# Performance work log

Measured on AMD Instinct MI355X. Metric: run time of the kernel, lower is better.

Reference implementation:

```python
import jax, jax.numpy as jnp
import numpy as np

Z_DIM = 3
H = 128
N_BLOCKS = 4
N = 30000
E = 180000
T = 2


def _mlp2(x, W1, b1, W2, b2):
    return jnp.maximum(x @ W1 + b1, 0.0) @ W2 + b2


def _stats(x, eps=1e-8):
    # batch mean/std as accumulated by the running-stat Normalizer (buffers -> no grad)
    m = x.mean(0)
    v = jnp.maximum((x * x).mean(0) - m * m, 0.0)
    s = jnp.maximum(jnp.sqrt(v), eps)
    return jax.lax.stop_gradient(m), jax.lax.stop_gradient(s)


def setup_inputs() -> dict:
    key = jax.random.key(0)
    ks = jax.random.split(key, 32)

    def w(k, shape, fan_in):
        return jax.random.normal(k, shape, jnp.float32) / np.sqrt(fan_in).astype(np.float32)

    inp = {}
    inp["z"] = jax.random.normal(ks[0], (T, N, Z_DIM), jnp.float32)
    inp["z_target"] = jax.random.normal(ks[1], (N, Z_DIM), jnp.float32)
    inp["pos"] = jax.random.uniform(ks[2], (N, 2), jnp.float32)
    # encoder node MLP: z_dim -> H -> H
    inp["enc_node_W1"] = w(ks[3], (Z_DIM, H), Z_DIM)
    inp["enc_node_b1"] = jnp.zeros((H,), jnp.float32)
    inp["enc_node_W2"] = w(ks[4], (H, H), H)
    inp["enc_node_b2"] = jnp.zeros((H,), jnp.float32)
    # encoder edge MLP: edge_dim(3) -> H -> H
    inp["enc_edge_W1"] = w(ks[5], (3, H), 3)
    inp["enc_edge_b1"] = jnp.zeros((H,), jnp.float32)
    inp["enc_edge_W2"] = w(ks[6], (H, H), H)
    inp["enc_edge_b2"] = jnp.zeros((H,), jnp.float32)
    # decoder MLP: H -> H -> z_dim
    inp["dec_W1"] = w(ks[7], (H, H), H)
    inp["dec_b1"] = jnp.zeros((H,), jnp.float32)
    inp["dec_W2"] = w(ks[8], (H, Z_DIM), H)
    inp["dec_b2"] = jnp.zeros((Z_DIM,), jnp.float32)
    # GraphNetBlocks, stacked over n_blocks
    inp["blk_edge_W1"] = w(ks[9], (N_BLOCKS, 3 * H, H), 3 * H)
    inp["blk_edge_b1"] = jnp.zeros((N_BLOCKS, H), jnp.float32)
    inp["blk_edge_W2"] = w(ks[10], (N_BLOCKS, H, H), H)
    inp["blk_edge_b2"] = jnp.zeros((N_BLOCKS, H), jnp.float32)
    inp["blk_node_W1"] = w(ks[11], (N_BLOCKS, 2 * H, H), 2 * H)
    inp["blk_node_b1"] = jnp.zeros((N_BLOCKS, H), jnp.float32)
    inp["blk_node_W2"] = w(ks[12], (N_BLOCKS, H, H), H)
    inp["blk_node_b2"] = jnp.zeros((N_BLOCKS, H), jnp.float32)
    # bidirectional mesh edges (triangles_to_edges output)
    inp["senders"] = jax.random.randint(ks[13], (E,), 0, N, jnp.int64)
    inp["receivers"] = jax.random.randint(ks[14], (E,), 0, N, jnp.int64)
    return inp


def reference(z, z_target, pos,
              enc_node_W1, enc_node_b1, enc_node_W2, enc_node_b2,
              enc_edge_W1, enc_edge_b1, enc_edge_W2, enc_edge_b2,
              dec_W1, dec_b1, dec_W2, dec_b2,
              blk_edge_W1, blk_edge_b1, blk_edge_W2, blk_edge_b2,
              blk_node_W1, blk_node_b1, blk_node_W2, blk_node_b2,
              senders, receivers):
    zl = z[-1]                                   # [N, z_dim]
    n_nodes = zl.shape[0]

    # --- build_graph ---
    rel = pos[senders] - pos[receivers]          # [E, 2]
    ef_raw = jnp.concatenate([rel, jnp.linalg.norm(rel, axis=1, keepdims=True)], axis=1)  # [E, 3]
    em, es = _stats(ef_raw)
    ef = _mlp2((ef_raw - em) / es, enc_edge_W1, enc_edge_b1, enc_edge_W2, enc_edge_b2)    # [E, H]
    nm, ns = _stats(zl)
    nf = _mlp2((zl - nm) / ns, enc_node_W1, enc_node_b1, enc_node_W2, enc_node_b2)        # [N, H]

    # --- message passing blocks ---
    def block(carry, p):
        nf, ef = carry
        eW1, eb1, eW2, eb2, nW1, nb1, nW2, nb2 = p
        e_in = jnp.concatenate([ef, nf[senders], nf[receivers]], axis=1)   # [E, 3H]
        ef = _mlp2(e_in, eW1, eb1, eW2, eb2) + ef
        agg = jax.ops.segment_sum(ef, receivers, num_segments=n_nodes)    # [N, H]
        n_in = jnp.concatenate([nf, agg], axis=1)                          # [N, 2H]
        nf = _mlp2(n_in, nW1, nb1, nW2, nb2) + nf
        return (nf, ef), None

    (nf, ef), _ = jax.lax.scan(block, (nf, ef),
                               (blk_edge_W1, blk_edge_b1, blk_edge_W2, blk_edge_b2,
                                blk_node_W1, blk_node_b1, blk_node_W2, blk_node_b2))

    # --- decode + loss ---
    output = _mlp2(nf, dec_W1, dec_b1, dec_W2, dec_b2)                     # [N, z_dim]
    target = z_target - zl
    om, os = _stats(target)
    target_normalized = (target - om) / os
    loss = jnp.mean((target_normalized - output) ** 2)

    z_update = jax.lax.stop_gradient(output) * os + om                     # Normalizer.inverse(detach)
    z_pred = zl + z_update
    rmse = jnp.mean(jnp.sqrt(jnp.mean((z_pred - z_target) ** 2, axis=0)))
    return z_pred, loss, rmse
```

## Files before the change

### kernel.cpp

```cpp
#include <hip/hip_runtime.h>
#include <hip/hip_bf16.h>
#include <math.h>

#define HDIM 128
#define TPB 256

typedef __attribute__((ext_vector_type(8))) short bf16x8;
typedef __attribute__((ext_vector_type(4))) float f32x4;

static inline int ceil_div(int a, int b){ return (a + b - 1) / b; }

__device__ __forceinline__ float wave_sum(float v){
#pragma unroll
  for (int o = 32; o > 0; o >>= 1) v += __shfl_down(v, o, 64);
  return v;
}
__device__ __forceinline__ int wave_sum_i(int v){
#pragma unroll
  for (int o = 32; o > 0; o >>= 1) v += __shfl_down(v, o, 64);
  return v;
}

__device__ __forceinline__ short f2bf(float f){
  __hip_bfloat16 h = __float2bfloat16(f);
  return *reinterpret_cast<short*>(&h);
}
__device__ __forceinline__ float bfb2f(short s){
  unsigned int u = ((unsigned int)(unsigned short)s) << 16;
  return __builtin_bit_cast(float, u);
}

__device__ __forceinline__ void gl_lds16(const short* g, short* l){
  __builtin_amdgcn_global_load_lds(
      (const __attribute__((address_space(1))) void*)g,
      (__attribute__((address_space(3))) void*)l, 16, 0, 0);
}

__global__ void csr_hist(const int* __restrict__ rcv, int* __restrict__ deg, int E){
  int e = blockIdx.x * blockDim.x + threadIdx.x;
  if (e < E) atomicAdd(&deg[rcv[e]], 1);
}

__global__ void scan_pass1(const int* __restrict__ deg, int* __restrict__ bsum, int N){
  __shared__ int red[4];
  int tid = threadIdx.x;
  int base = blockIdx.x * 1024;
  int s = 0;
  for (int i = tid; i < 1024; i += 256){
    int idx = base + i;
    if (idx < N) s += deg[idx];
  }
  s = wave_sum_i(s);
  if ((tid & 63) == 0) red[tid >> 6] = s;
  __syncthreads();
  if (tid == 0) bsum[blockIdx.x] = red[0] + red[1] + red[2] + red[3];
}

__global__ void scan_pass2(const int* __restrict__ bsum, int* __restrict__ boff,
                           int nb, int* __restrict__ row_start, int N, int E){
  if (threadIdx.x == 0){
    int acc = 0;
    for (int b = 0; b < nb; b++){ boff[b] = acc; acc += bsum[b]; }
    row_start[N] = E;
  }
}

__global__ void scan_pass3(const int* __restrict__ deg, const int* __restrict__ boff,
                           int* __restrict__ row_start, int* __restrict__ cursor, int N){
  __shared__ int tsum[256];
  int tid = threadIdx.x;
  int base = blockIdx.x * 1024;
  int i0 = base + tid * 4;
  int v[4];
  int s = 0;
#pragma unroll
  for (int k = 0; k < 4; k++){
    int idx = i0 + k;
    v[k] = (idx < N) ? deg[idx] : 0;
    s += v[k];
  }
  tsum[tid] = s;
  __syncthreads();
  for (int off = 1; off < 256; off <<= 1){
    int val = (tid >= off) ? tsum[tid - off] : 0;
    __syncthreads();
    tsum[tid] += val;
    __syncthreads();
  }
  int excl = (tid == 0) ? 0 : tsum[tid - 1];
  int b = boff[blockIdx.x] + excl;
#pragma unroll
  for (int k = 0; k < 4; k++){
    int idx = i0 + k;
    if (idx < N){
      row_start[idx] = b;
      cursor[idx]    = b;
      b += v[k];
    }
  }
}

__global__ void edge_prep(const float* __restrict__ pos,
                          const int* __restrict__ snd,
                          const int* __restrict__ rcv,
                          int* __restrict__ cursor,
// ... 18 lines not shown
    ef_raw[3*p+2] = nm;
    s[0] = rx; s[1] = ry; s[2] = nm;
    s[3] = rx*rx; s[4] = ry*ry; s[5] = nm*nm;
  }
#pragma unroll
  for (int k = 0; k < 6; k++) s[k] = wave_sum(s[k]);
  if (l == 0)
#pragma unroll
    for (int k = 0; k < 6; k++) red[w][k] = s[k];
  __syncthreads();
  if (tid < 6)
    epart[(size_t)blockIdx.x * 6 + tid] =
      red[0][tid] + red[1][tid] + red[2][tid] + red[3][tid];
}

__global__ void node_stats(const float* __restrict__ zl,
                           const float* __restrict__ z_target,
                           float* __restrict__ npart, int N){
  __shared__ float red[4][12];
  int tid = threadIdx.x, w = tid >> 6, l = tid & 63;
  int n = blockIdx.x * blockDim.x + tid;
  float s[12];
#pragma unroll
  for (int i = 0; i < 12; i++) s[i] = 0.f;
  if (n < N){
#pragma unroll
    for (int d = 0; d < 3; d++){
      float z = zl[3*n+d];
      float t = z_target[3*n+d] - z;
      s[d]   = z;  s[3+d] = z*z;
      s[6+d] = t;  s[9+d] = t*t;
    }
  }
#pragma unroll
  for (int i = 0; i < 12; i++) s[i] = wave_sum(s[i]);
  if (l == 0)
#pragma unroll
    for (int i = 0; i < 12; i++) red[w][i] = s[i];
  __syncthreads();
  if (tid < 12)
    npart[(size_t)blockIdx.x * 12 + tid] =
      red[0][tid] + red[1][tid] + red[2][tid] + red[3][tid];
}

__global__ void reduce_finalize(const float* __restrict__ ep, int ne,
                                const float* __restrict__ np_, int nn,
                                float* __restrict__ fin, int E, int N){
  __shared__ float red[4];
  __shared__ float raw[18];
  int tid = threadIdx.x, w = tid >> 6, l = tid & 63;
  for (int j = 0; j < 6; j++){
    float s = 0.f;
    for (int b = tid; b < ne; b += 256) s += ep[(size_t)b * 6 + j];
    s = wave_sum(s);
    if (l == 0) red[w] = s;
    __syncthreads();
    if (tid == 0) raw[j] = red[0] + red[1] + red[2] + red[3];
    __syncthreads();
  }
// ... 9 lines not shown
  if (tid == 0){
#pragma unroll
    for (int d = 0; d < 3; d++){
      float cE = (float)E, cN = (float)N;
      float m, v;
      m = raw[0+d] / cE; v = fmaxf(raw[3+d]/cE - m*m, 0.f);
      fin[0+d] = m;  fin[3+d]  = fmaxf(sqrtf(v), 1e-8f);
      m = raw[6+d] / cN; v = fmaxf(raw[9+d]/cN - m*m, 0.f);
      fin[6+d] = m;  fin[9+d]  = fmaxf(sqrtf(v), 1e-8f);
      m = raw[12+d] / cN; v = fmaxf(raw[15+d]/cN - m*m, 0.f);
      fin[12+d] = m; fin[15+d] = fmaxf(sqrtf(v), 1e-8f);
    }
  }
}

__global__ void pack_weights(const float* __restrict__ encEW2,
                             const float* __restrict__ encNW2,
                             const float* __restrict__ decW1,
                             const float* __restrict__ beW1,
                             const float* __restrict__ beW2,
                             const float* __restrict__ bnW1,
                             const float* __restrict__ bnW2,
                             __hip_bfloat16* __restrict__ wp){
  int y = blockIdx.y;
  const float* src; __hip_bfloat16* dst; int K;
  if (y == 0){ src = encEW2; dst = wp;          K = 128; }
  else if (y == 1){ src = encNW2; dst = wp + 16384; K = 128; }
  else if (y == 2){ src = decW1;  dst = wp + 32768; K = 128; }
  else {
    int b = (y - 3) >> 2, j = (y - 3) & 3;
    __hip_bfloat16* base = wp + 49152 + b * 114688;
    if (j == 0){ src = beW1 + b*49152; dst = base;          K = 384; }
    else if (j == 1){ src = beW2 + b*16384; dst = base + 49152; K = 128; }
    else if (j == 2){ src = bnW1 + b*32768; dst = base + 65536; K = 256; }
    else { src = bnW2 + b*16384; dst = base + 98304; K = 128; }
  }
  int id = blockIdx.x * blockDim.x + threadIdx.x;
  if (id >= 128 * K) return;
  int c = id >> 12;
  int r = id & 4095;
  int t = r >> 9;
  int l = (r >> 3) & 63;
  int j = r & 7;
  int k = c * 32 + ((l >> 4) << 3) + j;
  int n = t * 16 + (l & 15);
  dst[id] = __float2bfloat16(src[k * 128 + n]);
}

__launch_bounds__(256)
__global__ void encoder_fused(const float* __restrict__ raw,
                              const float* __restrict__ mptr,
                              const float* __restrict__ sptr,
                              const float* __restrict__ W1,
                              const float* __restrict__ b1,
                              const __hip_bfloat16* __restrict__ W2f,
                              const float* __restrict__ b2,
                              __hip_bfloat16* __restrict__ out, int rows){
  __shared__ __align__(16) short bsh[16384];
  const int tid = threadIdx.x, w = tid >> 6, l = tid & 63, m = l & 15, q = l >> 4;
  const short* wsrc = (const short*)W2f;
#pragma unroll
  for (int i = 0; i < 8; i++){
    int inst = w * 8 + i;
    gl_lds16(wsrc + inst * 512 + l * 8, &bsh[inst * 512]);
  }
  float s0 = mptr[0], s1 = mptr[1], s2 = mptr[2];
  float d0 = sptr[0], d1 = sptr[1], d2 = sptr[2];
  const int row0 = blockIdx.x * 64 + w * 16;
  const int ra = min(row0 + m, rows - 1);
  float x0 = (raw[3*ra]   - s0) / d0;
  float x1 = (raw[3*ra+1] - s1) / d1;
  float x2 = (raw[3*ra+2] - s2) / d2;
  bf16x8 afr[4];
#pragma unroll
  for (int c = 0; c < 4; c++){
    int nb = c * 32 + q * 8;
#pragma unroll
    for (int j = 0; j < 8; j++){
      float h = b1[nb+j] + x0 * W1[nb+j] + x1 * W1[128+nb+j] + x2 * W1[256+nb+j];
      afr[c][j] = f2bf(fmaxf(h, 0.f));
    }
  }
  f32x4 acc[8];
// ... 10 lines not shown
  }
  const int row_d = row0 + q * 4;
#pragma unroll
  for (int t = 0; t < 8; t++){
    int col = t * 16 + m;
    float bb = b2[col];
#pragma unroll
    for (int r = 0; r < 4; r++){
      int e = row_d + r;
      if (e < rows) out[(size_t)e * HDIM + col] = __float2bfloat16(acc[t][r] + bb);
    }
  }
}

__launch_bounds__(256)
__global__ void gemm128_g(const __hip_bfloat16* __restrict__ A,
                          const __hip_bfloat16* __restrict__ Wf,
                          const float* __restrict__ bias,
                          float* __restrict__ out, int rows){
  __shared__ __align__(16) short bsh[16384];
  const int tid = threadIdx.x, w = tid >> 6, l = tid & 63, m = l & 15, q = l >> 4;
  const short* wsrc = (const short*)Wf;
#pragma unroll
  for (int i = 0; i < 8; i++){
    int inst = w * 8 + i;
    gl_lds16(wsrc + inst * 512 + l * 8, &bsh[inst * 512]);
  }
  const int row0 = blockIdx.x * 64 + w * 16;
  const int ra = min(row0 + m, rows - 1);
  const short* pa = (const short*)A + (size_t)ra * HDIM + q * 8;
  bf16x8 afr[4];
#pragma unroll
  for (int c = 0; c < 4; c++) afr[c] = *(const bf16x8*)(pa + c * 32);
  f32x4 acc[8];
#pragma unroll
  for (int t = 0; t < 8; t++) acc[t] = (f32x4){0.f,0.f,0.f,0.f};
  __syncthreads();
#pragma unroll
  for (int c = 0; c < 4; c++){
#pragma unroll
    for (int t = 0; t < 8; t++){
      bf16x8 b = *(const bf16x8*)&bsh[(c*8 + t)*512 + l*8];
      acc[t] = __builtin_amdgcn_mfma_f32_16x16x32_bf16(afr[c], b, acc[t], 0, 0, 0);
    }
  }
  const int row_d = row0 + q * 4;
#pragma unroll
  for (int t = 0; t < 8; t++){
    int col = t * 16 + m;
    float bb = bias[col];
#pragma unroll
    for (int r = 0; r < 4; r++){
      int e = row_d + r;
      if (e < rows) out[(size_t)e * HDIM + col] = fmaxf(acc[t][r] + bb, 0.f);
    }
  }
}

__launch_bounds__(256)
__global__ void msg_pre(const __hip_bfloat16* __restrict__ nf,
                        const __hip_bfloat16* __restrict__ eWf,
                        __hip_bfloat16* __restrict__ u, int N){
  __shared__ __align__(16) short wsh[32768];
  const int tid = threadIdx.x, w = tid >> 6, l = tid & 63, m = l & 15, q = l >> 4;
  const short* wsrc = (const short*)eWf + 4 * 4096;
#pragma unroll
  for (int i = 0; i < 16; i++){
    int inst = i * 4 + w;
    gl_lds16(wsrc + inst * 512 + l * 8, &wsh[inst * 512]);
  }
  const int row0 = blockIdx.x * 64 + w * 16;
  const int ra = min(row0 + m, N - 1);
  const short* pa = (const short*)nf + (size_t)ra * HDIM + q * 8;
  bf16x8 afr[4];
#pragma unroll
  for (int c = 0; c < 4; c++) afr[c] = *(const bf16x8*)(pa + c * 32);
  f32x4 acc[16];
#pragma unroll
  for (int t = 0; t < 16; t++) acc[t] = (f32x4){0.f,0.f,0.f,0.f};
  __syncthreads();
#pragma unroll
  for (int c = 0; c < 4; c++){
#pragma unroll
    for (int t = 0; t < 16; t++){
      int cc = (t < 8) ? c : (4 + c);
      bf16x8 b = *(const bf16x8*)&wsh[cc * 4096 + (t & 7) * 512 + l * 8];
      acc[t] = __builtin_amdgcn_mfma_f32_16x16x32_bf16(afr[c], b, acc[t], 0, 0, 0);
    }
  }
  const int row_d = row0 + q * 4;
#pragma unroll
  for (int t = 0; t < 16; t++){
    int col = t * 16 + m;
#pragma unroll
    for (int r = 0; r < 4; r++){
      int n = row_d + r;
      if (n < N) u[(size_t)n * 256 + col] = __float2bfloat16(acc[t][r]);
    }
  }
}

__launch_bounds__(512)
__global__ void edge_block(const int* __restrict__ psnd,
                           const int* __restrict__ prcv,
                           const __hip_bfloat16* __restrict__ u,
                           __hip_bfloat16* __restrict__ ef,
                           const __hip_bfloat16* __restrict__ Wfrag,
                           const float* __restrict__ b1,
                           const float* __restrict__ b2,
                           int E){
  __shared__ __align__(16) short bsh[16384];
  __shared__ __align__(16) short hsh[8][16][136];
  const int tid = threadIdx.x, w = tid >> 6, l = tid & 63, m = l & 15, q = l >> 4;
  const short* wsrc = (const short*)Wfrag;
#pragma unroll
  for (int i = 0; i < 4; i++){
    int inst = i * 8 + w;
    gl_lds16(wsrc + inst * 512 + l * 8, &bsh[inst * 512]);
  }
  const int row0 = blockIdx.x * 128 + w * 16;
  const int ra = min(row0 + m, E - 1);
  const short* pe = (const short*)ef + (size_t)ra * HDIM + q * 8;
  bf16x8 afr[4];
#pragma unroll
  for (int c = 0; c < 4; c++) afr[c] = *(const bf16x8*)(pe + c * 32);

  {
    int grow = min(row0 + (l >> 2), E - 1);
    int us_row = psnd[grow], ur_row = prcv[grow];
    const short* pus = (const short*)u + (size_t)us_row * 256 + (l & 3) * 32;
    const short* pur = (const short*)u + (size_t)ur_row * 256 + 128 + (l & 3) * 32;
    short* hdst = &hsh[w][l >> 2][(l & 3) * 32];
#pragma unroll
    for (int k = 0; k < 4; k++){
      bf16x8 a = *(const bf16x8*)(pus + k * 8);
      bf16x8 b = *(const bf16x8*)(pur + k * 8);
      bf16x8 s;
#pragma unroll
      for (int j = 0; j < 8; j++) s[j] = f2bf(bfb2f(a[j]) + bfb2f(b[j]));
      *(bf16x8*)(hdst + k * 8) = s;
    }
  }
  f32x4 acc[8];
#pragma unroll
  for (int t = 0; t < 8; t++) acc[t] = (f32x4){0.f,0.f,0.f,0.f};
  __syncthreads();
#pragma unroll
  for (int c = 0; c < 4; c++){
#pragma unroll
    for (int t = 0; t < 8; t++){
      bf16x8 b = *(const bf16x8*)&bsh[(c*8 + t)*512 + l*8];
      acc[t] = __builtin_amdgcn_mfma_f32_16x16x32_bf16(afr[c], b, acc[t], 0, 0, 0);
    }
  }
  __syncthreads();
#pragma unroll
  for (int i = 0; i < 4; i++){
    int inst = i * 8 + w;
    gl_lds16(wsrc + 49152 + inst * 512 + l * 8, &bsh[inst * 512]);
  }
#pragma unroll
  for (int t = 0; t < 8; t++){
    float bb = b1[t * 16 + m];
#pragma unroll
    for (int r = 0; r < 4; r++){
      float uval = bfb2f(hsh[w][q*4 + r][t*16 + m]);
      hsh[w][q*4 + r][t*16 + m] = f2bf(fmaxf(acc[t][r] + uval + bb, 0.f));
    }
  }
  __syncthreads();
  const short* ph = &hsh[w][m][0] + q * 8;
#pragma unroll
  for (int t = 0; t < 8; t++) acc[t] = (f32x4){0.f,0.f,0.f,0.f};
#pragma unroll
  for (int c = 0; c < 4; c++){
    bf16x8 a = *(const bf16x8*)(ph + c * 32);
#pragma unroll
    for (int t = 0; t < 8; t++){
      bf16x8 b = *(const bf16x8*)&bsh[(c*8 + t)*512 + l*8];
      acc[t] = __builtin_amdgcn_mfma_f32_16x16x32_bf16(a, b, acc[t], 0, 0, 0);
    }
  }
#pragma unroll
  for (int t = 0; t < 8; t++){
    float bb = b2[t * 16 + m];
#pragma unroll
    for (int r = 0; r < 4; r++)
      hsh[w][q*4 + r][t*16 + m] = f2bf(acc[t][r] + bb);
  }
  const int orow = row0 + (l >> 2);
  if (orow < E){
    const short* pold = (const short*)ef + (size_t)orow * HDIM + (l & 3) * 32;
    const short* src = &hsh[w][l >> 2][(l & 3) * 32];
    short* dst = (short*)ef + (size_t)orow * HDIM + (l & 3) * 32;
#pragma unroll
    for (int k = 0; k < 4; k++){
      bf16x8 vnew = *(const bf16x8*)(src + k * 8);
      bf16x8 vo   = *(const bf16x8*)(pold + k * 8);
      bf16x8 vr;
#pragma unroll
      for (int j = 0; j < 8; j++) vr[j] = f2bf(bfb2f(vnew[j]) + bfb2f(vo[j]));
      *(bf16x8*)(dst + k * 8) = vr;
    }
  }
}

#define NB_COMPUTE_CHUNK(c) do {                                               \
  const short* bb_ = &bsh[(((c) >> 1) & 1) * 8192 + ((c) & 1) * 4096];         \
  _Pragma("unroll")                                                            \
  for (int t = 0; t < 8; t++){                                                 \
    bf16x8 b = *(const bf16x8*)(bb_ + t * 512 + l * 8);                        \
    acc[t] = __builtin_amdgcn_mfma_f32_16x16x32_bf16(afr[c], b, acc[t], 0, 0, 0); \
  }                                                                            \
} while(0)

__launch_bounds__(256)
// ... 100 lines not shown
    const short* pold = (const short*)nf + (size_t)orow * HDIM + (l & 3) * 32;
    const short* src = &hsh[w][l >> 2][(l & 3) * 32];
    short* dst = (short*)nf + (size_t)orow * HDIM + (l & 3) * 32;
#pragma unroll
    for (int k = 0; k < 4; k++){
      bf16x8 vnew = *(const bf16x8*)(src + k * 8);
      bf16x8 vo   = *(const bf16x8*)(pold + k * 8);
      bf16x8 vr;
#pragma unroll
      for (int j = 0; j < 8; j++) vr[j] = f2bf(bfb2f(vnew[j]) + bfb2f(vo[j]));
      *(bf16x8*)(dst + k * 8) = vr;
    }
  }
}

__global__ void dec_final(const float* __restrict__ hbuf,
                          const float* __restrict__ W2,
                          const float* __restrict__ b2,
                          float* __restrict__ outd, int rows){
  __shared__ float hl[64 * 129];
  __shared__ float Wl[HDIM * 3];
  __shared__ float bl[3];
  int t = threadIdx.x;
  int node0 = blockIdx.x * 64;
  for (int i = t; i < HDIM * 3; i += 256) Wl[i] = W2[i];
  if (t < 3) bl[t] = b2[t];
#pragma unroll
  for (int i = 0; i < 32; i++){
    int lin = t + i * 256;
    int r = lin >> 7;
    int c = lin & 127;
    int node = node0 + r;
    hl[r * 129 + c] = (node < rows) ? hbuf[(size_t)node * HDIM + c] : 0.f;
  }
  __syncthreads();
  if (t < 64){
    int node = node0 + t;
    if (node < rows){
      float a0 = bl[0], a1 = bl[1], a2 = bl[2];
      for (int k = 0; k < HDIM; k++){
        float v = hl[t * 129 + k];
        a0 += v * Wl[k * 3];
        a1 += v * Wl[k * 3 + 1];
        a2 += v * Wl[k * 3 + 2];
      }
      outd[3 * node]     = a0;
      outd[3 * node + 1] = a1;
      outd[3 * node + 2] = a2;
    }
  }
}

__global__ void epilogue(const float* __restrict__ dec_out,
                         const float* __restrict__ zl,
                         const float* __restrict__ z_target,
                         const float* __restrict__ fin,
                         float* __restrict__ d_out,
                         float* __restrict__ lpart, int N){
  __shared__ float red[4][4];
  int tid = threadIdx.x, w = tid >> 6, l = tid & 63;
  int n = blockIdx.x * blockDim.x + tid;
  float s[4] = {0.f,0.f,0.f,0.f};
  if (n < N){
#pragma unroll
    for (int d = 0; d < 3; d++){
      float om = fin[12 + d], os = fin[15 + d];
      float o   = dec_out[3*n + d];
      float zld = zl[3*n + d];
      float zt  = z_target[3*n + d];
      float tgt = zt - zld;
      float tn  = (tgt - om) / os;
      float diff = tn - o;
      s[0] += diff * diff;
      float zp = zld + o * os + om;
      d_out[3*n + d] = zp;
      float e = zp - zt;
      s[1 + d] = e * e;
    }
  }
#pragma unroll
  for (int k = 0; k < 4; k++) s[k] = wave_sum(s[k]);
  if (l == 0)
#pragma unroll
    for (int k = 0; k < 4; k++) red[w][k] = s[k];
  __syncthreads();
  if (tid < 4)
    lpart[(size_t)blockIdx.x * 4 + tid] =
      red[0][tid] + red[1][tid] + red[2][tid] + red[3][tid];
}

__global__ void finalize_out(const float* __restrict__ lpart, int nb,
                             float* __restrict__ d_out, int N){
  __shared__ float red[4];
  __shared__ float vals[4];
  int tid = threadIdx.x, w = tid >> 6, l = tid & 63;
  for (int j = 0; j < 4; j++){
    float s = 0.f;
    for (int b = tid; b < nb; b += 256) s += lpart[(size_t)b * 4 + j];
    s = wave_sum(s);
    if (l == 0) red[w] = s;
    __syncthreads();
    if (tid == 0) vals[j] = red[0] + red[1] + red[2] + red[3];
    __syncthreads();
  }
  if (tid == 0){
    float cN = (float)N;
    float loss = vals[0] / (3.f * cN);
    float rmse = (sqrtf(vals[1] / cN) + sqrtf(vals[2] / cN) + sqrtf(vals[3] / cN)) / 3.f;
    d_out[(size_t)3 * N]     = loss;
    d_out[(size_t)3 * N + 1] = rmse;
  }
}

extern "C" void kernel_launch(void* const* d_in, const int* in_sizes, int n_in,
                              void* d_out, int out_size, void* d_ws, size_t ws_size,
                              hipStream_t stream){
  const float* z           = (const float*)d_in[0];
  const float* z_target    = (const float*)d_in[1];
  const float* pos         = (const float*)d_in[2];
  const float* enc_node_W1 = (const float*)d_in[3];
  const float* enc_node_b1 = (const float*)d_in[4];
  const float* enc_node_W2 = (const float*)d_in[5];
  const float* enc_node_b2 = (const float*)d_in[6];
  const float* enc_edge_W1 = (const float*)d_in[7];
  const float* enc_edge_b1 = (const float*)d_in[8];
// ... 9 lines not shown
  const float* blk_edge_b2 = (const float*)d_in[18];
  const float* blk_node_W1 = (const float*)d_in[19];
  const float* blk_node_b1 = (const float*)d_in[20];
  const float* blk_node_W2 = (const float*)d_in[21];
  const float* blk_node_b2 = (const float*)d_in[22];
  const int*   senders     = (const int*)d_in[23];
  const int*   receivers   = (const int*)d_in[24];

  const int N = in_sizes[1] / 3;
  const int E = in_sizes[23];
  const float* zl = z + (size_t)N * 3;

  const int neb = ceil_div(E, TPB);
  const int nnb = ceil_div(N, TPB);
  const int nsb = ceil_div(N, 1024);

  char* p = (char*)d_ws;
  auto carve = [&](size_t bytes) -> char* {
    char* r = p; p += (bytes + 255) & ~(size_t)255; return r;
  };
  float* stats_fin = (float*)carve(32 * 4);
  float* epart     = (float*)carve((size_t)neb * 6 * 4);
  float* npart     = (float*)carve((size_t)nnb * 12 * 4);
  float* lpart     = (float*)carve((size_t)nnb * 4 * 4);
  float* ef_raw    = (float*)carve((size_t)E * 3 * 4);
  float* dec_out   = (float*)carve((size_t)N * 3 * 4);
  float* hbuf      = (float*)carve((size_t)N * HDIM * 4);
  int*   deg       = (int*)carve((size_t)N * 4);
  int*   bsum      = (int*)carve((size_t)(nsb + 1) * 4);
  int*   boff      = (int*)carve((size_t)(nsb + 1) * 4);
  int*   row_start = (int*)carve((size_t)(N + 1) * 4);
  int*   cursor    = (int*)carve((size_t)N * 4);
  int*   psnd      = (int*)carve((size_t)E * 4);
  int*   prcv      = (int*)carve((size_t)E * 4);
  __hip_bfloat16* wp = (__hip_bfloat16*)carve((size_t)507904 * 2);
  __hip_bfloat16* ef = (__hip_bfloat16*)carve((size_t)E * HDIM * 2);
  __hip_bfloat16* nf = (__hip_bfloat16*)carve((size_t)N * HDIM * 2);
  __hip_bfloat16* u  = (__hip_bfloat16*)carve((size_t)N * 256 * 2);

  float* out = (float*)d_out;

  hipMemsetAsync(deg, 0, (size_t)N * 4, stream);

  csr_hist<<<neb, TPB, 0, stream>>>(receivers, deg, E);
  scan_pass1<<<nsb, TPB, 0, stream>>>(deg, bsum, N);
  scan_pass2<<<1, 64, 0, stream>>>(bsum, boff, nsb, row_start, N, E);
  scan_pass3<<<nsb, TPB, 0, stream>>>(deg, boff, row_start, cursor, N);
  edge_prep<<<neb, TPB, 0, stream>>>(pos, senders, receivers, cursor,
                                     psnd, prcv, ef_raw, epart, E);

  node_stats<<<nnb, TPB, 0, stream>>>(zl, z_target, npart, N);
  reduce_finalize<<<1, TPB, 0, stream>>>(epart, neb, npart, nnb, stats_fin, E, N);

  pack_weights<<<dim3(192, 19), TPB, 0, stream>>>(enc_edge_W2, enc_node_W2, dec_W1,
                                                  blk_edge_W1, blk_edge_W2,
                                                  blk_node_W1, blk_node_W2, wp);

  encoder_fused<<<ceil_div(E, 64), TPB, 0, stream>>>(ef_raw, stats_fin + 0, stats_fin + 3,
                                                     enc_edge_W1, enc_edge_b1,
                                                     wp, enc_edge_b2, ef, E);
  encoder_fused<<<ceil_div(N, 64), TPB, 0, stream>>>(zl, stats_fin + 6, stats_fin + 9,
                                                     enc_node_W1, enc_node_b1,
                                                     wp + 16384, enc_node_b2, nf, N);

  for (int b = 0; b < 4; b++){
    const __hip_bfloat16* eWf = wp + 49152 + (size_t)b * 114688;
    const __hip_bfloat16* nWf = eWf + 65536;
    const float* eb1 = blk_edge_b1 + (size_t)b * 128;
    const float* eb2 = blk_edge_b2 + (size_t)b * 128;
    const float* nb1 = blk_node_b1 + (size_t)b * 128;
    const float* nb2 = blk_node_b2 + (size_t)b * 128;

    msg_pre<<<ceil_div(N, 64), 256, 0, stream>>>(nf, eWf, u, N);
    edge_block<<<ceil_div(E, 128), 512, 0, stream>>>(psnd, prcv, u, ef,
                                                     eWf, eb1, eb2, E);
    node_block<<<ceil_div(N, 64), 256, 0, stream>>>(row_start, ef, nf,
                                                    nWf, nb1, nb2, N);
  }

  gemm128_g<<<ceil_div(N, 64), TPB, 0, stream>>>(nf, wp + 32768, dec_b1, hbuf, N);
  dec_final<<<ceil_div(N, 64), TPB, 0, stream>>>(hbuf, dec_W2, dec_b2, dec_out, N);

  epilogue<<<nnb, TPB, 0, stream>>>(dec_out, zl, z_target, stats_fin,
                                    out, lpart, N);
  finalize_out<<<1, TPB, 0, stream>>>(lpart, nnb, out, N);
}
```

Before: 500.8 us.

## Merge prep and encoder launches, fuse decoder tail, and shrink LDS in block kernels

Cuts the launch count in several places. The CSR histogram, node stats and weight packing now run as one kernel, and scan_pass2 is folded into scan_pass3. The two encoder launches become one, and the decoder GEMM, final projection, epilogue and loss finalize become a single kernel that uses atomics and a last-block counter. msg_pre and edge_block stage half as much weight in LDS at a time, reloading in chunks, and edge_block gains a launch-bounds occupancy hint. The aim is lower launch overhead and higher occupancy, at the cost of extra syncs, serial prefix sums per block, and float atomics that can make the loss accumulation order nondeterministic.

New measurement: 522.6 us. 1.04x slower.

```diff
diff --git a/kernel.cpp b/kernel.cpp
--- a/kernel.cpp
+++ b/kernel.cpp
@@ -36,9 +36,76 @@
       (__attribute__((address_space(3))) void*)l, 16, 0, 0);
 }
 
-__global__ void csr_hist(const int* __restrict__ rcv, int* __restrict__ deg, int E){
-  int e = blockIdx.x * blockDim.x + threadIdx.x;
-  if (e < E) atomicAdd(&deg[rcv[e]], 1);
+__global__ void prep_a(const int* __restrict__ rcv, int* __restrict__ deg, int E, int neb,
+                       const float* __restrict__ zl, const float* __restrict__ zt,
+                       float* __restrict__ npart, int N, int nnb,
+                       const float* __restrict__ encEW2,
+                       const float* __restrict__ encNW2,
+                       const float* __restrict__ decW1,
+                       const float* __restrict__ beW1,
+                       const float* __restrict__ beW2,
+                       const float* __restrict__ bnW1,
+                       const float* __restrict__ bnW2,
+                       __hip_bfloat16* __restrict__ wp){
+  __shared__ float red[4][12];
+  const int bx = blockIdx.x, tid = threadIdx.x;
+  if (bx < neb){
+    int e = bx * 256 + tid;
+    if (e < E) atomicAdd(&deg[rcv[e]], 1);
+    return;
+  }
+  if (bx < neb + nnb){
+    int b = bx - neb;
+    int w = tid >> 6, l = tid & 63;
+    int n = b * 256 + tid;
+    float s[12];
+#pragma unroll
+    for (int i = 0; i < 12; i++) s[i] = 0.f;
+    if (n < N){
+#pragma unroll
+      for (int d = 0; d < 3; d++){
+        float z = zl[3*n+d];
+        float t = zt[3*n+d] - z;
+        s[d]   = z;  s[3+d] = z*z;
+        s[6+d] = t;  s[9+d] = t*t;
+      }
+    }
+#pragma unroll
+    for (int i = 0; i < 12; i++) s[i] = wave_sum(s[i]);
+    if (l == 0)
+#pragma unroll
+      for (int i = 0; i < 12; i++) red[w][i] = s[i];
+    __syncthreads();
+    if (tid < 12)
+      npart[(size_t)b * 12 + tid] =
+        red[0][tid] + red[1][tid] + red[2][tid] + red[3][tid];
+    return;
+  }
+  int pid = bx - neb - nnb;
+  int y = pid / 192;
+  int x = pid - y * 192;
+  const float* src; __hip_bfloat16* dst; int K;
+  if (y == 0){ src = encEW2; dst = wp;          K = 128; }
+  else if (y == 1){ src = encNW2; dst = wp + 16384; K = 128; }
+  else if (y == 2){ src = decW1;  dst = wp + 32768; K = 128; }
+  else {
+    int b = (y - 3) >> 2, j = (y - 3) & 3;
+    __hip_bfloat16* base = wp + 49152 + b * 114688;
+    if (j == 0){ src = beW1 + b*49152; dst = base;          K = 384; }
+    else if (j == 1){ src = beW2 + b*16384; dst = base + 49152; K = 128; }
+    else if (j == 2){ src = bnW1 + b*32768; dst = base + 65536; K = 256; }
+    else { src = bnW2 + b*16384; dst = base + 98304; K = 128; }
+  }
+  int id = x * 256 + tid;
+  if (id >= 128 * K) return;
+  int c = id >> 12;
+  int r = id & 4095;
+  int t = r >> 9;
+  int l = (r >> 3) & 63;
+  int j = r & 7;
+  int k = c * 32 + ((l >> 4) << 3) + j;
+  int n = t * 16 + (l & 15);
+  dst[id] = __float2bfloat16(src[k * 128 + n]);
 }
 
 __global__ void scan_pass1(const int* __restrict__ deg, int* __restrict__ bsum, int N){
@@ -56,19 +123,18 @@
   if (tid == 0) bsum[blockIdx.x] = red[0] + red[1] + red[2] + red[3];
 }
 
-__global__ void scan_pass2(const int* __restrict__ bsum, int* __restrict__ boff,
-                           int nb, int* __restrict__ row_start, int N, int E){
-  if (threadIdx.x == 0){
+__global__ void scan_pass3(const int* __restrict__ deg, const int* __restrict__ bsum,
+                           int nsb, int* __restrict__ row_start,
+                           int* __restrict__ cursor, int N, int E){
+  __shared__ int tsum[256];
+  __shared__ int base_s;
+  int tid = threadIdx.x;
+  if (tid == 0){
     int acc = 0;
-    for (int b = 0; b < nb; b++){ boff[b] = acc; acc += bsum[b]; }
-    row_start[N] = E;
-  }
-}
-
-__global__ void scan_pass3(const int* __restrict__ deg, const int* __restrict__ boff,
-                           int* __restrict__ row_start, int* __restrict__ cursor, int N){
-  __shared__ int tsum[256];
-  int tid = threadIdx.x;
+    for (int b = 0; b < (int)blockIdx.x; b++) acc += bsum[b];
+    base_s = acc;
+    if (blockIdx.x == 0) row_start[N] = E;
+  }
   int base = blockIdx.x * 1024;
   int i0 = base + tid * 4;
   int v[4];
@@ -88,7 +154,7 @@
     __syncthreads();
   }
   int excl = (tid == 0) ? 0 : tsum[tid - 1];
-  int b = boff[blockIdx.x] + excl;
+  int b = base_s + excl;
 #pragma unroll
   for (int k = 0; k < 4; k++){
     int idx = i0 + k;
@@ -137,35 +203,6 @@
       red[0][tid] + red[1][tid] + red[2][tid] + red[3][tid];
 }
 
-__global__ void node_stats(const float* __restrict__ zl,
-                           const float* __restrict__ z_target,
-                           float* __restrict__ npart, int N){
-  __shared__ float red[4][12];
-  int tid = threadIdx.x, w = tid >> 6, l = tid & 63;
-  int n = blockIdx.x * blockDim.x + tid;
-  float s[12];
-#pragma unroll
-  for (int i = 0; i < 12; i++) s[i] = 0.f;
-  if (n < N){
-#pragma unroll
-    for (int d = 0; d < 3; d++){
-      float z = zl[3*n+d];
-      float t = z_target[3*n+d] - z;
-      s[d]   = z;  s[3+d] = z*z;
-      s[6+d] = t;  s[9+d] = t*t;
-    }
-  }
-#pragma unroll
-  for (int i = 0; i < 12; i++) s[i] = wave_sum(s[i]);
-  if (l == 0)
-#pragma unroll
-    for (int i = 0; i < 12; i++) red[w][i] = s[i];
-  __syncthreads();
-  if (tid < 12)
-    npart[(size_t)blockIdx.x * 12 + tid] =
-      red[0][tid] + red[1][tid] + red[2][tid] + red[3][tid];
-}
-
 __global__ void reduce_finalize(const float* __restrict__ ep, int ne,
                                 const float* __restrict__ np_, int nn,
                                 float* __restrict__ fin, int E, int N){
@@ -205,51 +242,29 @@
   }
 }
 
-__global__ void pack_weights(const float* __restrict__ encEW2,
-                             const float* __restrict__ encNW2,
-                             const float* __restrict__ decW1,
-                             const float* __restrict__ beW1,
-                             const float* __restrict__ beW2,
-                             const float* __restrict__ bnW1,
-                             const float* __restrict__ bnW2,
-                             __hip_bfloat16* __restrict__ wp){
-  int y = blockIdx.y;
-  const float* src; __hip_bfloat16* dst; int K;
-  if (y == 0){ src = encEW2; dst = wp;          K = 128; }
-  else if (y == 1){ src = encNW2; dst = wp + 16384; K = 128; }
-  else if (y == 2){ src = decW1;  dst = wp + 32768; K = 128; }
-  else {
-    int b = (y - 3) >> 2, j = (y - 3) & 3;
-    __hip_bfloat16* base = wp + 49152 + b * 114688;
-    if (j == 0){ src = beW1 + b*49152; dst = base;          K = 384; }
-    else if (j == 1){ src = beW2 + b*16384; dst = base + 49152; K = 128; }
-    else if (j == 2){ src = bnW1 + b*32768; dst = base + 65536; K = 256; }
-    else { src = bnW2 + b*16384; dst = base + 98304; K = 128; }
-  }
-  int id = blockIdx.x * blockDim.x + threadIdx.x;
-  if (id >= 128 * K) return;
-  int c = id >> 12;
-  int r = id & 4095;
-  int t = r >> 9;
-  int l = (r >> 3) & 63;
-  int j = r & 7;
-  int k = c * 32 + ((l >> 4) << 3) + j;
-  int n = t * 16 + (l & 15);
-  dst[id] = __float2bfloat16(src[k * 128 + n]);
-}
-
 __launch_bounds__(256)
-__global__ void encoder_fused(const float* __restrict__ raw,
-                              const float* __restrict__ mptr,
-                              const float* __restrict__ sptr,
-                              const float* __restrict__ W1,
-                              const float* __restrict__ b1,
-                              const __hip_bfloat16* __restrict__ W2f,
-                              const float* __restrict__ b2,
-                              __hip_bfloat16* __restrict__ out, int rows){
+__global__ void encoder_both(const float* __restrict__ eraw,
+                             const float* __restrict__ zl,
+                             const float* __restrict__ fin,
+                             const float* __restrict__ eW1, const float* __restrict__ eb1,
+                             const float* __restrict__ nW1, const float* __restrict__ nb1,
+                             const __hip_bfloat16* __restrict__ wp,
+                             const float* __restrict__ eb2, const float* __restrict__ nb2,
+                             __hip_bfloat16* __restrict__ efo, __hip_bfloat16* __restrict__ nfo,
+                             int E, int N, int EB){
   __shared__ __align__(16) short bsh[16384];
   const int tid = threadIdx.x, w = tid >> 6, l = tid & 63, m = l & 15, q = l >> 4;
-  const short* wsrc = (const short*)W2f;
+  const bool ise = ((int)blockIdx.x < EB);
+  const float* raw = ise ? eraw : zl;
+  const float* mptr = fin + (ise ? 0 : 6);
+  const float* sptr = fin + (ise ? 3 : 9);
+  const float* W1 = ise ? eW1 : nW1;
+  const float* b1 = ise ? eb1 : nb1;
+  const float* b2 = ise ? eb2 : nb2;
+  const short* wsrc = (const short*)wp + (ise ? 0 : 16384);
+  __hip_bfloat16* out = ise ? efo : nfo;
+  const int rows = ise ? E : N;
+  const int bx = ise ? (int)blockIdx.x : (int)blockIdx.x - EB;
 #pragma unroll
   for (int i = 0; i < 8; i++){
     int inst = w * 8 + i;
@@ -257,7 +272,7 @@
   }
   float s0 = mptr[0], s1 = mptr[1], s2 = mptr[2];
   float d0 = sptr[0], d1 = sptr[1], d2 = sptr[2];
-  const int row0 = blockIdx.x * 64 + w * 16;
+  const int row0 = bx * 64 + w * 16;
   const int ra = min(row0 + m, rows - 1);
   float x0 = (raw[3*ra]   - s0) / d0;
   float x1 = (raw[3*ra+1] - s1) / d1;
@@ -298,60 +313,16 @@
 }
 
 __launch_bounds__(256)
-__global__ void gemm128_g(const __hip_bfloat16* __restrict__ A,
-                          const __hip_bfloat16* __restrict__ Wf,
-                          const float* __restrict__ bias,
-                          float* __restrict__ out, int rows){
-  __shared__ __align__(16) short bsh[16384];
-  const int tid = threadIdx.x, w = tid >> 6, l = tid & 63, m = l & 15, q = l >> 4;
-  const short* wsrc = (const short*)Wf;
-#pragma unroll
-  for (int i = 0; i < 8; i++){
-    int inst = w * 8 + i;
-    gl_lds16(wsrc + inst * 512 + l * 8, &bsh[inst * 512]);
-  }
-  const int row0 = blockIdx.x * 64 + w * 16;
-  const int ra = min(row0 + m, rows - 1);
-  const short* pa = (const short*)A + (size_t)ra * HDIM + q * 8;
-  bf16x8 afr[4];
-#pragma unroll
-  for (int c = 0; c < 4; c++) afr[c] = *(const bf16x8*)(pa + c * 32);
-  f32x4 acc[8];
-#pragma unroll
-  for (int t = 0; t < 8; t++) acc[t] = (f32x4){0.f,0.f,0.f,0.f};
-  __syncthreads();
-#pragma unroll
-  for (int c = 0; c < 4; c++){
-#pragma unroll
-    for (int t = 0; t < 8; t++){
-      bf16x8 b = *(const bf16x8*)&bsh[(c*8 + t)*512 + l*8];
-      acc[t] = __builtin_amdgcn_mfma_f32_16x16x32_bf16(afr[c], b, acc[t], 0, 0, 0);
-    }
-  }
-  const int row_d = row0 + q * 4;
-#pragma unroll
-  for (int t = 0; t < 8; t++){
-    int col = t * 16 + m;
-    float bb = bias[col];
-#pragma unroll
-    for (int r = 0; r < 4; r++){
-      int e = row_d + r;
-      if (e < rows) out[(size_t)e * HDIM + col] = fmaxf(acc[t][r] + bb, 0.f);
-    }
-  }
-}
-
-__launch_bounds__(256)
 __global__ void msg_pre(const __hip_bfloat16* __restrict__ nf,
                         const __hip_bfloat16* __restrict__ eWf,
                         __hip_bfloat16* __restrict__ u, int N){
-  __shared__ __align__(16) short wsh[32768];
+  __shared__ __align__(16) short wsh[16384];
   const int tid = threadIdx.x, w = tid >> 6, l = tid & 63, m = l & 15, q = l >> 4;
   const short* wsrc = (const short*)eWf + 4 * 4096;
 #pragma unroll
-  for (int i = 0; i < 16; i++){
-    int inst = i * 4 + w;
-    gl_lds16(wsrc + inst * 512 + l * 8, &wsh[inst * 512]);
+  for (int i = 0; i < 8; i++){
+    int f = w * 8 + i;
+    gl_lds16(wsrc + f * 512 + l * 8, &wsh[f * 512]);
   }
   const int row0 = blockIdx.x * 64 + w * 16;
   const int ra = min(row0 + m, N - 1);
@@ -359,22 +330,20 @@
   bf16x8 afr[4];
 #pragma unroll
   for (int c = 0; c < 4; c++) afr[c] = *(const bf16x8*)(pa + c * 32);
-  f32x4 acc[16];
-#pragma unroll
-  for (int t = 0; t < 16; t++) acc[t] = (f32x4){0.f,0.f,0.f,0.f};
-  __syncthreads();
-#pragma unroll
-  for (int c = 0; c < 4; c++){
-#pragma unroll
-    for (int t = 0; t < 16; t++){
-      int cc = (t < 8) ? c : (4 + c);
-      bf16x8 b = *(const bf16x8*)&wsh[cc * 4096 + (t & 7) * 512 + l * 8];
+  f32x4 acc[8];
+#pragma unroll
+  for (int t = 0; t < 8; t++) acc[t] = (f32x4){0.f,0.f,0.f,0.f};
+  __syncthreads();
+#pragma unroll
+  for (int c = 0; c < 4; c++)
+#pragma unroll
+    for (int t = 0; t < 8; t++){
+      bf16x8 b = *(const bf16x8*)&wsh[(c*8 + t)*512 + l*8];
       acc[t] = __builtin_amdgcn_mfma_f32_16x16x32_bf16(afr[c], b, acc[t], 0, 0, 0);
     }
-  }
   const int row_d = row0 + q * 4;
 #pragma unroll
-  for (int t = 0; t < 16; t++){
+  for (int t = 0; t < 8; t++){
     int col = t * 16 + m;
 #pragma unroll
     for (int r = 0; r < 4; r++){
@@ -382,9 +351,34 @@
       if (n < N) u[(size_t)n * 256 + col] = __float2bfloat16(acc[t][r]);
     }
   }
-}
-
-__launch_bounds__(512)
+  __syncthreads();
+#pragma unroll
+  for (int i = 0; i < 8; i++){
+    int f = w * 8 + i;
+    gl_lds16(wsrc + 16384 + f * 512 + l * 8, &wsh[f * 512]);
+  }
+#pragma unroll
+  for (int t = 0; t < 8; t++) acc[t] = (f32x4){0.f,0.f,0.f,0.f};
+  __syncthreads();
+#pragma unroll
+  for (int c = 0; c < 4; c++)
+#pragma unroll
+    for (int t = 0; t < 8; t++){
+      bf16x8 b = *(const bf16x8*)&wsh[(c*8 + t)*512 + l*8];
+      acc[t] = __builtin_amdgcn_mfma_f32_16x16x32_bf16(afr[c], b, acc[t], 0, 0, 0);
+    }
+#pragma unroll
+  for (int t = 0; t < 8; t++){
+    int col = 128 + t * 16 + m;
+#pragma unroll
+    for (int r = 0; r < 4; r++){
+      int n = row_d + r;
+      if (n < N) u[(size_t)n * 256 + col] = __float2bfloat16(acc[t][r]);
+    }
+  }
+}
+
+__launch_bounds__(512, 6)
 __global__ void edge_block(const int* __restrict__ psnd,
                            const int* __restrict__ prcv,
                            const __hip_bfloat16* __restrict__ u,
@@ -393,25 +387,21 @@
                            const float* __restrict__ b1,
                            const float* __restrict__ b2,
                            int E){
-  __shared__ __align__(16) short bsh[16384];
+  __shared__ __align__(16) short bsh[8192];
   __shared__ __align__(16) short hsh[8][16][136];
   const int tid = threadIdx.x, w = tid >> 6, l = tid & 63, m = l & 15, q = l >> 4;
   const short* wsrc = (const short*)Wfrag;
-#pragma unroll
-  for (int i = 0; i < 4; i++){
-    int inst = i * 8 + w;
-    gl_lds16(wsrc + inst * 512 + l * 8, &bsh[inst * 512]);
-  }
   const int row0 = blockIdx.x * 128 + w * 16;
+  const int grow = min(row0 + (l >> 2), E - 1);
+  const int us_row = psnd[grow], ur_row = prcv[grow];
+  gl_lds16(wsrc + (w*2)  *512 + l*8, &bsh[(w*2)  *512]);
+  gl_lds16(wsrc + (w*2+1)*512 + l*8, &bsh[(w*2+1)*512]);
   const int ra = min(row0 + m, E - 1);
   const short* pe = (const short*)ef + (size_t)ra * HDIM + q * 8;
   bf16x8 afr[4];
 #pragma unroll
   for (int c = 0; c < 4; c++) afr[c] = *(const bf16x8*)(pe + c * 32);
-
   {
-    int grow = min(row0 + (l >> 2), E - 1);
-    int us_row = psnd[grow], ur_row = prcv[grow];
     const short* pus = (const short*)u + (size_t)us_row * 256 + (l & 3) * 32;
     const short* pur = (const short*)u + (size_t)ur_row * 256 + 128 + (l & 3) * 32;
     short* hdst = &hsh[w][l >> 2][(l & 3) * 32];
@@ -430,19 +420,26 @@
   for (int t = 0; t < 8; t++) acc[t] = (f32x4){0.f,0.f,0.f,0.f};
   __syncthreads();
 #pragma unroll
-  for (int c = 0; c < 4; c++){
+  for (int cc = 0; cc < 2; cc++)
 #pragma unroll
     for (int t = 0; t < 8; t++){
-      bf16x8 b = *(const bf16x8*)&bsh[(c*8 + t)*512 + l*8];
-      acc[t] = __builtin_amdgcn_mfma_f32_16x16x32_bf16(afr[c], b, acc[t], 0, 0, 0);
-    }
-  }
-  __syncthreads();
-#pragma unroll
-  for (int i = 0; i < 4; i++){
-    int inst = i * 8 + w;
-    gl_lds16(wsrc + 49152 + inst * 512 + l * 8, &bsh[inst * 512]);
-  }
+      bf16x8 b = *(const bf16x8*)&bsh[(cc*8 + t)*512 + l*8];
+      acc[t] = __builtin_amdgcn_mfma_f32_16x16x32_bf16(afr[cc], b, acc[t], 0, 0, 0);
+    }
+  __syncthreads();
+  gl_lds16(wsrc + 8192 + (w*2)  *512 + l*8, &bsh[(w*2)  *512]);
+  gl_lds16(wsrc + 8192 + (w*2+1)*512 + l*8, &bsh[(w*2+1)*512]);
+  __syncthreads();
+#pragma unroll
+  for (int cc = 0; cc < 2; cc++)
+#pragma unroll
+    for (int t = 0; t < 8; t++){
+      bf16x8 b = *(const bf16x8*)&bsh[(cc*8 + t)*512 + l*8];
+      acc[t] = __builtin_amdgcn_mfma_f32_16x16x32_bf16(afr[2+cc], b, acc[t], 0, 0, 0);
+    }
+  __syncthreads();
+  gl_lds16(wsrc + 49152 + (w*2)  *512 + l*8, &bsh[(w*2)  *512]);
+  gl_lds16(wsrc + 49152 + (w*2+1)*512 + l*8, &bsh[(w*2+1)*512]);
 #pragma unroll
   for (int t = 0; t < 8; t++){
     float bb = b1[t * 16 + m];
@@ -453,18 +450,36 @@
     }
   }
   __syncthreads();
+  bf16x8 ah[4];
   const short* ph = &hsh[w][m][0] + q * 8;
 #pragma unroll
+  for (int c = 0; c < 4; c++) ah[c] = *(const bf16x8*)(ph + c * 32);
+#pragma unroll
   for (int t = 0; t < 8; t++) acc[t] = (f32x4){0.f,0.f,0.f,0.f};
 #pragma unroll
-  for (int c = 0; c < 4; c++){
-    bf16x8 a = *(const bf16x8*)(ph + c * 32);
+  for (int cc = 0; cc < 2; cc++)
 #pragma unroll
     for (int t = 0; t < 8; t++){
-      bf16x8 b = *(const bf16x8*)&bsh[(c*8 + t)*512 + l*8];
-      acc[t] = __builtin_amdgcn_mfma_f32_16x16x32_bf16(a, b, acc[t], 0, 0, 0);
-    }
-  }
+      bf16x8 b = *(const bf16x8*)&bsh[(cc*8 + t)*512 + l*8];
+      acc[t] = __builtin_amdgcn_mfma_f32_16x16x32_bf16(ah[cc], b, acc[t], 0, 0, 0);
+    }
+  __syncthreads();
+  gl_lds16(wsrc + 57344 + (w*2)  *512 + l*8, &bsh[(w*2)  *512]);
+  gl_lds16(wsrc + 57344 + (w*2+1)*512 + l*8, &bsh[(w*2+1)*512]);
+  const int orow = row0 + (l >> 2);
+  const int orc = min(orow, E - 1);
+  const short* pold = (const short*)ef + (size_t)orc * HDIM + (l & 3) * 32;
+  bf16x8 vold[4];
+#pragma unroll
+  for (int k = 0; k < 4; k++) vold[k] = *(const bf16x8*)(pold + k * 8);
+  __syncthreads();
+#pragma unroll
+  for (int cc = 0; cc < 2; cc++)
+#pragma unroll
+    for (int t = 0; t < 8; t++){
+      bf16x8 b = *(const bf16x8*)&bsh[(cc*8 + t)*512 + l*8];
+      acc[t] = __builtin_amdgcn_mfma_f32_16x16x32_bf16(ah[2+cc], b, acc[t], 0, 0, 0);
+    }
 #pragma unroll
   for (int t = 0; t < 8; t++){
     float bb = b2[t * 16 + m];
@@ -472,18 +487,15 @@
     for (int r = 0; r < 4; r++)
       hsh[w][q*4 + r][t*16 + m] = f2bf(acc[t][r] + bb);
   }
-  const int orow = row0 + (l >> 2);
   if (orow < E){
-    const short* pold = (const short*)ef + (size_t)orow * HDIM + (l & 3) * 32;
     const short* src = &hsh[w][l >> 2][(l & 3) * 32];
     short* dst = (short*)ef + (size_t)orow * HDIM + (l & 3) * 32;
 #pragma unroll
     for (int k = 0; k < 4; k++){
       bf16x8 vnew = *(const bf16x8*)(src + k * 8);
-      bf16x8 vo   = *(const bf16x8*)(pold + k * 8);
       bf16x8 vr;
 #pragma unroll
-      for (int j = 0; j < 8; j++) vr[j] = f2bf(bfb2f(vnew[j]) + bfb2f(vo[j]));
+      for (int j = 0; j < 8; j++) vr[j] = f2bf(bfb2f(vnew[j]) + bfb2f(vold[k][j]));
       *(bf16x8*)(dst + k * 8) = vr;
     }
   }
@@ -614,68 +626,91 @@
   }
 }
 
-__global__ void dec_final(const float* __restrict__ hbuf,
+__launch_bounds__(256)
+__global__ void dec_fused(const __hip_bfloat16* __restrict__ A,
+                          const __hip_bfloat16* __restrict__ Wf,
+                          const float* __restrict__ b1,
                           const float* __restrict__ W2,
                           const float* __restrict__ b2,
-                          float* __restrict__ outd, int rows){
-  __shared__ float hl[64 * 129];
+                          const float* __restrict__ zl,
+                          const float* __restrict__ z_target,
+                          const float* __restrict__ fin,
+                          float* __restrict__ d_out,
+                          float* __restrict__ lred,
+                          unsigned int* __restrict__ cnt,
+                          int N){
+  __shared__ __align__(16) short bsh[16384];
   __shared__ float Wl[HDIM * 3];
-  __shared__ float bl[3];
-  int t = threadIdx.x;
-  int node0 = blockIdx.x * 64;
-  for (int i = t; i < HDIM * 3; i += 256) Wl[i] = W2[i];
-  if (t < 3) bl[t] = b2[t];
-#pragma unroll
-  for (int i = 0; i < 32; i++){
-    int lin = t + i * 256;
-    int r = lin >> 7;
-    int c = lin & 127;
-    int node = node0 + r;
-    hl[r * 129 + c] = (node < rows) ? hbuf[(size_t)node * HDIM + c] : 0.f;
-  }
-  __syncthreads();
-  if (t < 64){
-    int node = node0 + t;
-    if (node < rows){
-      float a0 = bl[0], a1 = bl[1], a2 = bl[2];
-      for (int k = 0; k < HDIM; k++){
-        float v = hl[t * 129 + k];
-        a0 += v * Wl[k * 3];
-        a1 += v * Wl[k * 3 + 1];
-        a2 += v * Wl[k * 3 + 2];
+  __shared__ float red[4][4];
+  const int tid = threadIdx.x, w = tid >> 6, l = tid & 63, m = l & 15, q = l >> 4;
+  const short* wsrc = (const short*)Wf;
+#pragma unroll
+  for (int i = 0; i < 8; i++){
+    int inst = w * 8 + i;
+    gl_lds16(wsrc + inst * 512 + l * 8, &bsh[inst * 512]);
+  }
+  for (int i = tid; i < HDIM * 3; i += 256) Wl[i] = W2[i];
+  const int row0 = blockIdx.x * 64 + w * 16;
+  const int ra = min(row0 + m, N - 1);
+  const short* pa = (const short*)A + (size_t)ra * HDIM + q * 8;
+  bf16x8 afr[4];
+#pragma unroll
+  for (int c = 0; c < 4; c++) afr[c] = *(const bf16x8*)(pa + c * 32);
+  f32x4 acc[8];
+#pragma unroll
+  for (int t = 0; t < 8; t++) acc[t] = (f32x4){0.f,0.f,0.f,0.f};
+  __syncthreads();
+#pragma unroll
+  for (int c = 0; c < 4; c++){
+#pragma unroll
+    for (int t = 0; t < 8; t++){
+      bf16x8 b = *(const bf16x8*)&bsh[(c*8 + t)*512 + l*8];
+      acc[t] = __builtin_amdgcn_mfma_f32_16x16x32_bf16(afr[c], b, acc[t], 0, 0, 0);
+    }
+  }
+  float p0[4] = {0,0,0,0}, p1[4] = {0,0,0,0}, p2[4] = {0,0,0,0};
+#pragma unroll
+  for (int t = 0; t < 8; t++){
+    int col = t * 16 + m;
+    float bb = b1[col];
+    float w0 = Wl[col*3], w1 = Wl[col*3+1], w2 = Wl[col*3+2];
+#pragma unroll
+    for (int r = 0; r < 4; r++){
+      float h = fmaxf(acc[t][r] + bb, 0.f);
+      p0[r] += h * w0; p1[r] += h * w1; p2[r] += h * w2;
+    }
+  }
+#pragma unroll
+  for (int r = 0; r < 4; r++){
+#pragma unroll
+    for (int o = 1; o < 16; o <<= 1){
+      p0[r] += __shfl_xor(p0[r], o, 64);
+      p1[r] += __shfl_xor(p1[r], o, 64);
+      p2[r] += __shfl_xor(p2[r], o, 64);
+    }
+  }
+  float s[4] = {0.f,0.f,0.f,0.f};
+  if (m == 0){
+#pragma unroll
+    for (int r = 0; r < 4; r++){
+      int n = row0 + q * 4 + r;
+      if (n < N){
+        float pd[3] = {p0[r], p1[r], p2[r]};
+#pragma unroll
+        for (int d = 0; d < 3; d++){
+          float o   = pd[d] + b2[d];
+          float om = fin[12 + d], os = fin[15 + d];
+          float zld = zl[3*n + d];
+          float zt  = z_target[3*n + d];
+          float tn  = ((zt - zld) - om) / os;
+          float diff = tn - o;
+          s[0] += diff * diff;
+          float zp = zld + o * os + om;
+          d_out[3*n + d] = zp;
+          float e = zp - zt;
+          s[1 + d] += e * e;
+        }
       }
-      outd[3 * node]     = a0;
-      outd[3 * node + 1] = a1;
-      outd[3 * node + 2] = a2;
-    }
-  }
-}
-
-__global__ void epilogue(const float* __restrict__ dec_out,
-                         const float* __restrict__ zl,
-                         const float* __restrict__ z_target,
-                         const float* __restrict__ fin,
-                         float* __restrict__ d_out,
-                         float* __restrict__ lpart, int N){
-  __shared__ float red[4][4];
-  int tid = threadIdx.x, w = tid >> 6, l = tid & 63;
-  int n = blockIdx.x * blockDim.x + tid;
-  float s[4] = {0.f,0.f,0.f,0.f};
-  if (n < N){
-#pragma unroll
-    for (int d = 0; d < 3; d++){
-      float om = fin[12 + d], os = fin[15 + d];
-      float o   = dec_out[3*n + d];
-      float zld = zl[3*n + d];
-      float zt  = z_target[3*n + d];
-      float tgt = zt - zld;
-      float tn  = (tgt - om) / os;
-      float diff = tn - o;
-      s[0] += diff * diff;
-      float zp = zld + o * os + om;
-      d_out[3*n + d] = zp;
-      float e = zp - zt;
-      s[1 + d] = e * e;
     }
   }
 #pragma unroll
@@ -685,30 +720,21 @@
     for (int k = 0; k < 4; k++) red[w][k] = s[k];
   __syncthreads();
   if (tid < 4)
-    lpart[(size_t)blockIdx.x * 4 + tid] =
-      red[0][tid] + red[1][tid] + red[2][tid] + red[3][tid];
-}
-
-__global__ void finalize_out(const float* __restrict__ lpart, int nb,
-                             float* __restrict__ d_out, int N){
-  __shared__ float red[4];
-  __shared__ float vals[4];
-  int tid = threadIdx.x, w = tid >> 6, l = tid & 63;
-  for (int j = 0; j < 4; j++){
-    float s = 0.f;
-    for (int b = tid; b < nb; b += 256) s += lpart[(size_t)b * 4 + j];
-    s = wave_sum(s);
-    if (l == 0) red[w] = s;
-    __syncthreads();
-    if (tid == 0) vals[j] = red[0] + red[1] + red[2] + red[3];
-    __syncthreads();
-  }
+    atomicAdd(&lred[tid], red[0][tid] + red[1][tid] + red[2][tid] + red[3][tid]);
+  __syncthreads();
   if (tid == 0){
-    float cN = (float)N;
-    float loss = vals[0] / (3.f * cN);
-    float rmse = (sqrtf(vals[1] / cN) + sqrtf(vals[2] / cN) + sqrtf(vals[3] / cN)) / 3.f;
-    d_out[(size_t)3 * N]     = loss;
-    d_out[(size_t)3 * N + 1] = rmse;
+    __threadfence();
+    unsigned int t = atomicAdd(cnt, 1u);
+    if (t == gridDim.x - 1){
+      float vals[4];
+#pragma unroll
+      for (int k = 0; k < 4; k++) vals[k] = atomicAdd(&lred[k], 0.f);
+      float cN = (float)N;
+      float loss = vals[0] / (3.f * cN);
+      float rmse = (sqrtf(vals[1]/cN) + sqrtf(vals[2]/cN) + sqrtf(vals[3]/cN)) / 3.f;
+      d_out[(size_t)3 * N]     = loss;
+      d_out[(size_t)3 * N + 1] = rmse;
+    }
   }
 }
 
@@ -748,6 +774,8 @@
   const int neb = ceil_div(E, TPB);
   const int nnb = ceil_div(N, TPB);
   const int nsb = ceil_div(N, 1024);
+  const int EB  = ceil_div(E, 64);
+  const int NB  = ceil_div(N, 64);
 
   char* p = (char*)d_ws;
   auto carve = [&](size_t bytes) -> char* {
@@ -756,13 +784,11 @@
   float* stats_fin = (float*)carve(32 * 4);
   float* epart     = (float*)carve((size_t)neb * 6 * 4);
   float* npart     = (float*)carve((size_t)nnb * 12 * 4);
-  float* lpart     = (float*)carve((size_t)nnb * 4 * 4);
   float* ef_raw    = (float*)carve((size_t)E * 3 * 4);
-  float* dec_out   = (float*)carve((size_t)N * 3 * 4);
-  float* hbuf      = (float*)carve((size_t)N * HDIM * 4);
-  int*   deg       = (int*)carve((size_t)N * 4);
+  int*   deg       = (int*)carve((size_t)(N + 16) * 4);
+  float* lred      = (float*)(deg + N);
+  unsigned int* cnt = (unsigned int*)(deg + N + 4);
   int*   bsum      = (int*)carve((size_t)(nsb + 1) * 4);
-  int*   boff      = (int*)carve((size_t)(nsb + 1) * 4);
   int*   row_start = (int*)carve((size_t)(N + 1) * 4);
   int*   cursor    = (int*)carve((size_t)N * 4);
   int*   psnd      = (int*)carve((size_t)E * 4);
@@ -774,28 +800,24 @@
 
   float* out = (float*)d_out;
 
-  hipMemsetAsync(deg, 0, (size_t)N * 4, stream);
-
-  csr_hist<<<neb, TPB, 0, stream>>>(receivers, deg, E);
+  hipMemsetAsync(deg, 0, (size_t)(N + 16) * 4, stream);
+
+  prep_a<<<neb + nnb + 3648, TPB, 0, stream>>>(receivers, deg, E, neb,
+                                               zl, z_target, npart, N, nnb,
+                                               enc_edge_W2, enc_node_W2, dec_W1,
+                                               blk_edge_W1, blk_edge_W2,
+                                               blk_node_W1, blk_node_W2, wp);
   scan_pass1<<<nsb, TPB, 0, stream>>>(deg, bsum, N);
-  scan_pass2<<<1, 64, 0, stream>>>(bsum, boff, nsb, row_start, N, E);
-  scan_pass3<<<nsb, TPB, 0, stream>>>(deg, boff, row_start, cursor, N);
+  scan_pass3<<<nsb, TPB, 0, stream>>>(deg, bsum, nsb, row_start, cursor, N, E);
   edge_prep<<<neb, TPB, 0, stream>>>(pos, senders, receivers, cursor,
                                      psnd, prcv, ef_raw, epart, E);
-
-  node_stats<<<nnb, TPB, 0, stream>>>(zl, z_target, npart, N);
   reduce_finalize<<<1, TPB, 0, stream>>>(epart, neb, npart, nnb, stats_fin, E, N);
 
-  pack_weights<<<dim3(192, 19), TPB, 0, stream>>>(enc_edge_W2, enc_node_W2, dec_W1,
-                                                  blk_edge_W1, blk_edge_W2,
-                                                  blk_node_W1, blk_node_W2, wp);
-
-  encoder_fused<<<ceil_div(E, 64), TPB, 0, stream>>>(ef_raw, stats_fin + 0, stats_fin + 3,
-                                                     enc_edge_W1, enc_edge_b1,
-                                                     wp, enc_edge_b2, ef, E);
-  encoder_fused<<<ceil_div(N, 64), TPB, 0, stream>>>(zl, stats_fin + 6, stats_fin + 9,
-                                                     enc_node_W1, enc_node_b1,
-                                                     wp + 16384, enc_node_b2, nf, N);
+  encoder_both<<<EB + NB, TPB, 0, stream>>>(ef_raw, zl, stats_fin,
+                                            enc_edge_W1, enc_edge_b1,
+                                            enc_node_W1, enc_node_b1,
+                                            wp, enc_edge_b2, enc_node_b2,
+                                            ef, nf, E, N, EB);
 
   for (int b = 0; b < 4; b++){
     const __hip_bfloat16* eWf = wp + 49152 + (size_t)b * 114688;
@@ -805,17 +827,14 @@
     const float* nb1 = blk_node_b1 + (size_t)b * 128;
     const float* nb2 = blk_node_b2 + (size_t)b * 128;
 
-    msg_pre<<<ceil_div(N, 64), 256, 0, stream>>>(nf, eWf, u, N);
+    msg_pre<<<NB, TPB, 0, stream>>>(nf, eWf, u, N);
     edge_block<<<ceil_div(E, 128), 512, 0, stream>>>(psnd, prcv, u, ef,
                                                      eWf, eb1, eb2, E);
-    node_block<<<ceil_div(N, 64), 256, 0, stream>>>(row_start, ef, nf,
-                                                    nWf, nb1, nb2, N);
-  }
-
-  gemm128_g<<<ceil_div(N, 64), TPB, 0, stream>>>(nf, wp + 32768, dec_b1, hbuf, N);
-  dec_final<<<ceil_div(N, 64), TPB, 0, stream>>>(hbuf, dec_W2, dec_b2, dec_out, N);
-
-  epilogue<<<nnb, TPB, 0, stream>>>(dec_out, zl, z_target, stats_fin,
-                                    out, lpart, N);
-  finalize_out<<<1, TPB, 0, stream>>>(lpart, nnb, out, N);
-}
+    node_block<<<NB, TPB, 0, stream>>>(row_start, ef, nf,
+                                       nWf, nb1, nb2, N);
+  }
+
+  dec_fused<<<NB, TPB, 0, stream>>>(nf, wp + 32768, dec_b1, dec_W2, dec_b2,
+                                    zl, z_target, stats_fin,
+                                    out, lred, cnt, N);
+}
```
